# Optimization experiments

Hardware: AMD Instinct MI355X
Metric: run time of the kernel (lower is better)

## Reference

```python
import jax, jax.numpy as jnp
import numpy as np

CONV = 332.07156


def setup_inputs() -> dict:
    key = jax.random.key(0)
    ks = jax.random.split(key, 6)
    B, N, C = 4, 2048, 32
    X = jax.random.normal(ks[0], (B, N, 3), dtype=jnp.float32) * 5.0
    embs = jax.random.uniform(ks[1], (B, N, C), dtype=jnp.float32)
    qs = jax.random.normal(ks[2], (B, N), dtype=jnp.float32)
    paired_mask = jnp.zeros((B, N, N), dtype=bool)
    # learned parameters, initialized as in the torch module
    Born_factor = jax.random.normal(ks[3], (C,), dtype=jnp.float32) * 0.1 + 1.0
    die_factor = jax.random.normal(ks[4], (C,), dtype=jnp.float32) * 0.1 + 4.0
    screening_filter = jax.random.normal(ks[5], (2 * C + 1, 1), dtype=jnp.float32) * 0.1
    screening_filter = screening_filter.at[-1, :].set(1.0)
    return {"X": X, "embs": embs, "qs": qs, "paired_mask": paired_mask,
            "Born_factor": Born_factor, "die_factor": die_factor,
            "screening_filter": screening_filter}


def reference(X, embs, qs, paired_mask, Born_factor, die_factor, screening_filter):
    B, N, _ = X.shape
    C = embs.shape[-1]
    # all-pairs displacement and distance; note +1e-6 added per component before sum
    V = X[:, None, :, :] - X[:, :, None, :]            # (B,N,N,3)
    D = jnp.sqrt(jnp.sum(V * V + 1e-6, axis=-1))       # (B,N,N)
    invD = 1.0 / (D + 1e-6)
    # per-atom Born / dielectric scalars
    atomic_die = embs @ die_factor + 1e-6               # (B,N)
    R = embs @ Born_factor + 1.0                        # (B,N)
    E_self = -(1.0 - 1.0 / atomic_die) * qs / (R + 1e-6)  # (B,N)
    # pairwise screening: cat([emb_i, emb_j, D]) @ filter, algebraically separable
    w_i = screening_filter[:C, 0]                       # (C,)
    w_j = screening_filter[C:2 * C, 0]                  # (C,)
    w_d = screening_filter[2 * C, 0]                    # scalar
    s_i = embs @ w_i                                    # (B,N)
    s_j = embs @ w_j                                    # (B,N)
    screening = s_i[:, :, None] + s_j[:, None, :] + w_d * D  # (B,N,N)
    E_pair = invD * screening                           # (B,N,N)
    Etotal = CONV * (E_self.sum(axis=1) + 0.5 * E_pair.sum(axis=(1, 2))) * 0.01
    Etotal = jnp.where(jnp.isnan(Etotal), jnp.float32(1e-6), Etotal)
    return Etotal
```

## Files before the change

### kernel.cpp

```cpp
#include <hip/hip_runtime.h>
#include <math.h>

#define NB 4
#define NA 2048
#define NC 32
#define IT 256
#define UI 2
#define ITILE (IT * UI)
#define NS 64
#define JT (NA / NS)
#define NI (NA / ITILE)
#define SLOTS_PER_B (NI * NS)

static constexpr float CONV001 = 3.3207156f;


__global__ void __launch_bounds__(IT)
pair_kernel(const float* __restrict__ X,
            const float* __restrict__ embs,
            const float* __restrict__ qs,
            const float* __restrict__ born,
            const float* __restrict__ die,
            const float* __restrict__ sf,
            float* __restrict__ ws) {
    const int b  = blockIdx.z;
    const int t  = threadIdx.x;
    const int i0 = blockIdx.y * ITILE;
    const int j0 = blockIdx.x * JT;

    const float* Xb = X + (size_t)b * NA * 3;
    const float* Eb = embs + (size_t)b * NA * NC;

    __shared__ float4 jd[JT];

    if (t < JT) {
        int j = j0 + t;
        const float4* e4 = (const float4*)(Eb + (size_t)j * NC);
        float sj = 0.f;
        #pragma unroll
        for (int c = 0; c < NC / 4; ++c) {
            float4 ev = e4[c];
            sj = fmaf(ev.x, sf[NC + 4 * c + 0],
                 fmaf(ev.y, sf[NC + 4 * c + 1],
                 fmaf(ev.z, sf[NC + 4 * c + 2],
                 fmaf(ev.w, sf[NC + 4 * c + 3], sj))));
        }
        jd[t] = make_float4(Xb[j * 3 + 0], Xb[j * 3 + 1], Xb[j * 3 + 2], sj);
    }

    float xi[UI], yi[UI], zi[UI], si[UI], acc[UI];
    #pragma unroll
    for (int u = 0; u < UI; ++u) {
        int i = i0 + u * IT + t;
        const float4* e4 = (const float4*)(Eb + (size_t)i * NC);
        float s = 0.f;
        #pragma unroll
        for (int c = 0; c < NC / 4; ++c) {
            float4 ev = e4[c];
            s = fmaf(ev.x, sf[4 * c + 0],
                fmaf(ev.y, sf[4 * c + 1],
                fmaf(ev.z, sf[4 * c + 2],
                fmaf(ev.w, sf[4 * c + 3], s))));
        }
        si[u] = s;
        xi[u] = Xb[i * 3 + 0];
        yi[u] = Xb[i * 3 + 1];
        zi[u] = Xb[i * 3 + 2];
        acc[u] = 0.f;

        if (blockIdx.x == 0) {
            float ad = 0.f, R = 0.f;
            #pragma unroll
            for (int c = 0; c < NC / 4; ++c) {
                float4 ev = e4[c];
                ad = fmaf(ev.x, die[4 * c + 0],
                     fmaf(ev.y, die[4 * c + 1],
                     fmaf(ev.z, die[4 * c + 2],
                     fmaf(ev.w, die[4 * c + 3], ad))));
                R  = fmaf(ev.x, born[4 * c + 0],
                     fmaf(ev.y, born[4 * c + 1],
                     fmaf(ev.z, born[4 * c + 2],
                     fmaf(ev.w, born[4 * c + 3], R))));
            }
            ad += 1e-6f;
            R  += 1.0f;
            float eself = -(1.0f - __builtin_amdgcn_rcpf(ad)) * qs[b * NA + i]
                          * __builtin_amdgcn_rcpf(R + 1e-6f);
            acc[u] = 2.0f * eself;
        }
    }
    __syncthreads();

    #pragma unroll 4
    for (int jj = 0; jj < JT; ++jj) {
        float4 v = jd[jj];
        #pragma unroll
        for (int u = 0; u < UI; ++u) {
            float dx = v.x - xi[u];
            float dy = v.y - yi[u];
            float dz = v.z - zi[u];
            float d2 = fmaf(dx, dx, fmaf(dy, dy, fmaf(dz, dz, 3e-6f)));
            acc[u] = fmaf(__builtin_amdgcn_rsqf(d2), si[u] + v.w, acc[u]);
        }
    }

    float a = 0.f;
    #pragma unroll
    for (int u = 0; u < UI; ++u) a += acc[u];
    #pragma unroll
    for (int off = 32; off > 0; off >>= 1)
        a += __shfl_down(a, off, 64);
    __shared__ float wsum[IT / 64];
    int lane = t & 63;
    int w = t >> 6;
    if (lane == 0) wsum[w] = a;
    __syncthreads();
    if (t == 0) {
        int slot = (b * NI + blockIdx.y) * NS + blockIdx.x;
        ws[slot] = wsum[0] + wsum[1] + wsum[2] + wsum[3];
    }
}

__global__ void __launch_bounds__(1024)
finalize_kernel(const float* __restrict__ ws,
                const float* __restrict__ sf,
                float* __restrict__ out) {
    int t = threadIdx.x;
    float v = ws[t];
    #pragma unroll
    for (int off = 32; off > 0; off >>= 1)
        v += __shfl_down(v, off, 64);
    __shared__ float wsum[16];
    if ((t & 63) == 0) wsum[t >> 6] = v;
    __syncthreads();
    if (t < NB) {
        float accb = wsum[4 * t] + wsum[4 * t + 1]
                   + wsum[4 * t + 2] + wsum[4 * t + 3];
        float wd = sf[2 * NC];
        float r = CONV001 * 0.5f * (accb + wd * (float)NA * (float)NA);
        out[t] = isnan(r) ? 1e-6f : r;
    }
}

extern "C" void kernel_launch(void* const* d_in, const int* in_sizes, int n_in,
                              void* d_out, int out_size, void* d_ws, size_t ws_size,
                              hipStream_t stream) {
    const float* X    = (const float*)d_in[0];
    const float* embs = (const float*)d_in[1];
    const float* qs   = (const float*)d_in[2];
    const float* born = (const float*)d_in[4];
    const float* die  = (const float*)d_in[5];
    const float* sf   = (const float*)d_in[6];
    float* ws  = (float*)d_ws;
    float* out = (float*)d_out;

    pair_kernel<<<dim3(NS, NI, NB), IT, 0, stream>>>(X, embs, qs,
                                                     born, die, sf, ws);
    finalize_kernel<<<1, 1024, 0, stream>>>(ws, sf, out);
}
```

Baseline: 110.6 us.

## Precompute per-atom projections in a separate kernel before pair loop

Adds an atom_kernel that computes, once per atom, the screening projections s_i and s_j, the self-energy term, and packed float4 position records, writing them to workspace. The pair kernel then only loads these packed records instead of recomputing the 32-wide embedding dot products for every tile. This removes redundant embedding reads and FMAs across the 64 j-slices, at the cost of an extra kernel launch and a global round trip through workspace.

```diff
diff --git a/kernel.cpp b/kernel.cpp
--- a/kernel.cpp
+++ b/kernel.cpp
@@ -4,109 +4,106 @@
 #define NB 4
 #define NA 2048
 #define NC 32
+#define NATOM (NB * NA)
 #define IT 256
 #define UI 2
 #define ITILE (IT * UI)
 #define NS 64
 #define JT (NA / NS)
 #define NI (NA / ITILE)
-#define SLOTS_PER_B (NI * NS)
 
 static constexpr float CONV001 = 3.3207156f;
 
+#define WS_PI   0
+#define WS_PJ   32768
+#define WS_PAIR 65536
+#define WS_SELF 66560
 
-__global__ void __launch_bounds__(IT)
-pair_kernel(const float* __restrict__ X,
+__global__ void __launch_bounds__(256)
+atom_kernel(const float* __restrict__ X,
             const float* __restrict__ embs,
             const float* __restrict__ qs,
             const float* __restrict__ born,
             const float* __restrict__ die,
             const float* __restrict__ sf,
             float* __restrict__ ws) {
+    const int a = blockIdx.x * 256 + threadIdx.x;
+    const float4* e4 = (const float4*)(embs + (size_t)a * NC);
+
+    float si = 0.f, sj = 0.f, ad = 0.f, R = 0.f;
+    #pragma unroll
+    for (int c = 0; c < NC / 4; ++c) {
+        float4 ev = e4[c];
+        si = fmaf(ev.x, sf[4 * c + 0], fmaf(ev.y, sf[4 * c + 1],
+             fmaf(ev.z, sf[4 * c + 2], fmaf(ev.w, sf[4 * c + 3], si))));
+        sj = fmaf(ev.x, sf[NC + 4 * c + 0], fmaf(ev.y, sf[NC + 4 * c + 1],
+             fmaf(ev.z, sf[NC + 4 * c + 2], fmaf(ev.w, sf[NC + 4 * c + 3], sj))));
+        ad = fmaf(ev.x, die[4 * c + 0], fmaf(ev.y, die[4 * c + 1],
+             fmaf(ev.z, die[4 * c + 2], fmaf(ev.w, die[4 * c + 3], ad))));
+        R  = fmaf(ev.x, born[4 * c + 0], fmaf(ev.y, born[4 * c + 1],
+             fmaf(ev.z, born[4 * c + 2], fmaf(ev.w, born[4 * c + 3], R))));
+    }
+    float x = X[a * 3 + 0];
+    float y = X[a * 3 + 1];
+    float z = X[a * 3 + 2];
+    float4* Pi = (float4*)(ws + WS_PI);
+    float4* Pj = (float4*)(ws + WS_PJ);
+    Pi[a] = make_float4(x, y, z, si);
+    Pj[a] = make_float4(x, y, z, sj);
+
+    ad += 1e-6f;
+    R  += 1.0f;
+    float eself = -(1.0f - __builtin_amdgcn_rcpf(ad)) * qs[a]
+                  * __builtin_amdgcn_rcpf(R + 1e-6f);
+
+    #pragma unroll
+    for (int off = 32; off > 0; off >>= 1)
+        eself += __shfl_down(eself, off, 64);
+    __shared__ float wsum[4];
+    int lane = threadIdx.x & 63;
+    int w = threadIdx.x >> 6;
+    if (lane == 0) wsum[w] = eself;
+    __syncthreads();
+    if (threadIdx.x == 0)
+        ws[WS_SELF + blockIdx.x] = wsum[0] + wsum[1] + wsum[2] + wsum[3];
+}
+
+__global__ void __launch_bounds__(IT)
+pair_kernel(const float* __restrict__ wsc,
+            float* __restrict__ ws) {
     const int b  = blockIdx.z;
     const int t  = threadIdx.x;
-    const int i0 = blockIdx.y * ITILE;
-    const int j0 = blockIdx.x * JT;
+    const int i0 = b * NA + blockIdx.y * ITILE;
+    const int j0 = b * NA + blockIdx.x * JT;
 
-    const float* Xb = X + (size_t)b * NA * 3;
-    const float* Eb = embs + (size_t)b * NA * NC;
+    const float4* Pi = (const float4*)(wsc + WS_PI);
+    const float4* Pj = (const float4*)(wsc + WS_PJ);
 
     __shared__ float4 jd[JT];
+    if (t < JT)
+        jd[t] = Pj[j0 + t];
 
-    if (t < JT) {
-        int j = j0 + t;
-        const float4* e4 = (const float4*)(Eb + (size_t)j * NC);
-        float sj = 0.f;
-        #pragma unroll
-        for (int c = 0; c < NC / 4; ++c) {
-            float4 ev = e4[c];
-            sj = fmaf(ev.x, sf[NC + 4 * c + 0],
-                 fmaf(ev.y, sf[NC + 4 * c + 1],
-                 fmaf(ev.z, sf[NC + 4 * c + 2],
-                 fmaf(ev.w, sf[NC + 4 * c + 3], sj))));
-        }
-        jd[t] = make_float4(Xb[j * 3 + 0], Xb[j * 3 + 1], Xb[j * 3 + 2], sj);
-    }
-
-    float xi[UI], yi[UI], zi[UI], si[UI], acc[UI];
+    float4 id[UI];
     #pragma unroll
-    for (int u = 0; u < UI; ++u) {
-        int i = i0 + u * IT + t;
-        const float4* e4 = (const float4*)(Eb + (size_t)i * NC);
-        float s = 0.f;
-        #pragma unroll
-        for (int c = 0; c < NC / 4; ++c) {
-            float4 ev = e4[c];
-            s = fmaf(ev.x, sf[4 * c + 0],
-                fmaf(ev.y, sf[4 * c + 1],
-                fmaf(ev.z, sf[4 * c + 2],
-                fmaf(ev.w, sf[4 * c + 3], s))));
-        }
-        si[u] = s;
-        xi[u] = Xb[i * 3 + 0];
-        yi[u] = Xb[i * 3 + 1];
-        zi[u] = Xb[i * 3 + 2];
-        acc[u] = 0.f;
-
-        if (blockIdx.x == 0) {
-            float ad = 0.f, R = 0.f;
-            #pragma unroll
-            for (int c = 0; c < NC / 4; ++c) {
-                float4 ev = e4[c];
-                ad = fmaf(ev.x, die[4 * c + 0],
-                     fmaf(ev.y, die[4 * c + 1],
-                     fmaf(ev.z, die[4 * c + 2],
-                     fmaf(ev.w, die[4 * c + 3], ad))));
-                R  = fmaf(ev.x, born[4 * c + 0],
-                     fmaf(ev.y, born[4 * c + 1],
-                     fmaf(ev.z, born[4 * c + 2],
-                     fmaf(ev.w, born[4 * c + 3], R))));
-            }
-            ad += 1e-6f;
-            R  += 1.0f;
-            float eself = -(1.0f - __builtin_amdgcn_rcpf(ad)) * qs[b * NA + i]
-                          * __builtin_amdgcn_rcpf(R + 1e-6f);
-            acc[u] = 2.0f * eself;
-        }
-    }
+    for (int u = 0; u < UI; ++u)
+        id[u] = Pi[i0 + u * IT + t];
     __syncthreads();
 
+    float acc[UI] = {0.f, 0.f};
     #pragma unroll 4
     for (int jj = 0; jj < JT; ++jj) {
         float4 v = jd[jj];
         #pragma unroll
         for (int u = 0; u < UI; ++u) {
-            float dx = v.x - xi[u];
-            float dy = v.y - yi[u];
-            float dz = v.z - zi[u];
+            float dx = v.x - id[u].x;
+            float dy = v.y - id[u].y;
+            float dz = v.z - id[u].z;
             float d2 = fmaf(dx, dx, fmaf(dy, dy, fmaf(dz, dz, 3e-6f)));
-            acc[u] = fmaf(__builtin_amdgcn_rsqf(d2), si[u] + v.w, acc[u]);
+            acc[u] = fmaf(__builtin_amdgcn_rsqf(d2), id[u].w + v.w, acc[u]);
         }
     }
 
-    float a = 0.f;
-    #pragma unroll
-    for (int u = 0; u < UI; ++u) a += acc[u];
+    float a = acc[0] + acc[1];
     #pragma unroll
     for (int off = 32; off > 0; off >>= 1)
         a += __shfl_down(a, off, 64);
@@ -117,7 +114,7 @@
     __syncthreads();
     if (t == 0) {
         int slot = (b * NI + blockIdx.y) * NS + blockIdx.x;
-        ws[slot] = wsum[0] + wsum[1] + wsum[2] + wsum[3];
+        ws[WS_PAIR + slot] = wsum[0] + wsum[1] + wsum[2] + wsum[3];
     }
 }
 
@@ -126,7 +123,7 @@
                 const float* __restrict__ sf,
                 float* __restrict__ out) {
     int t = threadIdx.x;
-    float v = ws[t];
+    float v = ws[WS_PAIR + t];
     #pragma unroll
     for (int off = 32; off > 0; off >>= 1)
         v += __shfl_down(v, off, 64);
@@ -134,10 +131,15 @@
     if ((t & 63) == 0) wsum[t >> 6] = v;
     __syncthreads();
     if (t < NB) {
-        float accb = wsum[4 * t] + wsum[4 * t + 1]
+        float pair = wsum[4 * t] + wsum[4 * t + 1]
                    + wsum[4 * t + 2] + wsum[4 * t + 3];
+        float self = 0.f;
+        #pragma unroll
+        for (int k = 0; k < 8; ++k)
+            self += ws[WS_SELF + t * 8 + k];
         float wd = sf[2 * NC];
-        float r = CONV001 * 0.5f * (accb + wd * (float)NA * (float)NA);
+        float r = CONV001 * 0.5f * (pair + 2.0f * self
+                                    + wd * (float)NA * (float)NA);
         out[t] = isnan(r) ? 1e-6f : r;
     }
 }
@@ -154,7 +156,7 @@
     float* ws  = (float*)d_ws;
     float* out = (float*)d_out;
 
-    pair_kernel<<<dim3(NS, NI, NB), IT, 0, stream>>>(X, embs, qs,
-                                                     born, die, sf, ws);
+    atom_kernel<<<NATOM / 256, 256, 0, stream>>>(X, embs, qs, born, die, sf, ws);
+    pair_kernel<<<dim3(NS, NI, NB), IT, 0, stream>>>(ws, ws);
     finalize_kernel<<<1, 1024, 0, stream>>>(ws, sf, out);
 }
```

Result: faster. 108.1 us (-2.3%).
